# Optimization experiments

Hardware: AMD Instinct MI355X
Metric: run time of the kernel (lower is better)

## Reference

```python
import jax, jax.numpy as jnp
import numpy as np

D_MODEL = 1024
NUM_EXPERTS = 64
TOP_K = 2
TEMPERATURE = 1.0


def setup_inputs() -> dict:
    key = jax.random.key(0)
    k1, k2, k3, k4 = jax.random.split(key, 4)
    mh_output = jax.random.normal(k1, (8, 4096, D_MODEL), dtype=jnp.float32)
    noise = jax.random.normal(k2, (8, 4096, NUM_EXPERTS), dtype=jnp.float32)  # randn_like sample, externalized
    # nn.Linear weights: shape [out, in], init normal(0, 0.02); biases zero
    W_route = jax.random.normal(k3, (NUM_EXPERTS, D_MODEL), dtype=jnp.float32) * 0.02
    b_route = jnp.zeros((NUM_EXPERTS,), dtype=jnp.float32)
    W_noise = jax.random.normal(k4, (NUM_EXPERTS, D_MODEL), dtype=jnp.float32) * 0.02
    b_noise = jnp.zeros((NUM_EXPERTS,), dtype=jnp.float32)
    return {"mh_output": mh_output, "noise": noise, "W_route": W_route,
            "b_route": b_route, "W_noise": W_noise, "b_noise": b_noise}


def reference(mh_output, noise, W_route, b_route, W_noise, b_noise):
    # logits = topkroute_linear(mh_output); noise_logits = noise_linear(mh_output)
    logits = jnp.einsum('bsd,ed->bse', mh_output, W_route) + b_route
    noise_logits = jnp.einsum('bsd,ed->bse', mh_output, W_noise) + b_noise
    # noisy logits = logits + temperature * randn * softplus(noise_logits)
    noisy = logits + TEMPERATURE * noise * jax.nn.softplus(noise_logits)
    # top-k, scatter into -inf, softmax  ==  softmax over top-k values scattered into zeros
    top_vals, indices = jax.lax.top_k(noisy, TOP_K)          # [b, s, k]
    probs_k = jax.nn.softmax(top_vals, axis=-1)              # softmax(-inf elsewhere) -> 0 elsewhere
    one_hot = jax.nn.one_hot(indices, NUM_EXPERTS, dtype=noisy.dtype)  # [b, s, k, E]
    router_output = jnp.sum(one_hot * probs_k[..., None], axis=-2)     # [b, s, E]
    return router_output, indices
```

## Files before the change

### kernel.cpp

```cpp
#include <hip/hip_runtime.h>
#include <hip/hip_bf16.h>
#include <math.h>


#define T_TOKENS 32768
#define D_MODEL  1024
#define NE       64
#define NCOL     128
#define M_TILE   32
#define KSTAGE   64
#define NSTAGE   16
#define CS_LD    68
#define OUT_IDX_BASE ((size_t)T_TOKENS * NE)
#define W_ELEMS  (NCOL * D_MODEL)

typedef short  bf16x8  __attribute__((ext_vector_type(8)));
typedef float  floatx4 __attribute__((ext_vector_type(4)));

__device__ __forceinline__ float softplus_f(float x) {
    return fmaxf(x, 0.f) + log1pf(expf(-fabsf(x)));
}

__device__ __forceinline__ void cvt8(const float4 a, const float4 b,
                                     int4* hi, int4* lo) {
    float v[8] = {a.x, a.y, a.z, a.w, b.x, b.y, b.z, b.w};
    int hw[4], lw[4];
    #pragma unroll
    for (int p = 0; p < 4; ++p) {
        float2 f2 = make_float2(v[2 * p], v[2 * p + 1]);
        __hip_bfloat162 h2 = __float22bfloat162_rn(f2);
        int u; __builtin_memcpy(&u, &h2, 4);
        float h0 = __uint_as_float(((unsigned)u) << 16);
        float h1 = __uint_as_float(((unsigned)u) & 0xFFFF0000u);
        float2 l2 = make_float2(v[2 * p] - h0, v[2 * p + 1] - h1);
        __hip_bfloat162 L2 = __float22bfloat162_rn(l2);
        int ul; __builtin_memcpy(&ul, &L2, 4);
        hw[p] = u; lw[p] = ul;
    }
    *hi = make_int4(hw[0], hw[1], hw[2], hw[3]);
    *lo = make_int4(lw[0], lw[1], lw[2], lw[3]);
}

__global__ __launch_bounds__(256) void prepack_w(
    const float* __restrict__ Wr, const float* __restrict__ Wn,
    short* __restrict__ Bh, short* __restrict__ Bl)
{
    int g   = blockIdx.x * 256 + threadIdx.x;
    int n   = g & 15;
    int kg  = (g >> 4) & 127;
    int t2  = g >> 11;
    int col = t2 * 16 + n;
    const float* src = (col < NE ? Wr + (size_t)col * D_MODEL
                                 : Wn + (size_t)(col - NE) * D_MODEL) + kg * 8;
    float4 a = *(const float4*)src;
    float4 b = *(const float4*)(src + 4);
    int4 hi, lo;
    cvt8(a, b, &hi, &lo);
    *(int4*)(Bh + (size_t)g * 8) = hi;
    *(int4*)(Bl + (size_t)g * 8) = lo;
}

__global__ __launch_bounds__(256, 4) void router_mfma(
    const float* __restrict__ A,
    const float* __restrict__ noise,
    const float* __restrict__ br,
    const float* __restrict__ bn,
    const short* __restrict__ Bh,
    const short* __restrict__ Bl,
    float* __restrict__ out)
{
    __shared__ __align__(16) short Ah[2][M_TILE * KSTAGE];
    __shared__ __align__(16) short Al[2][M_TILE * KSTAGE];
    __shared__ float Cs[M_TILE * CS_LD];
    __shared__ float s_p1[M_TILE], s_p2[M_TILE];
    __shared__ int   s_e1[M_TILE], s_e2[M_TILE];

    const int tid  = threadIdx.x;
    const int lane = tid & 63;
    const int wid  = tid >> 6;
    const int n16  = lane & 15;
    const int quad = lane >> 4;
    const int m0   = blockIdx.x * M_TILE;

    const int r  = tid & 31;
    const int kh = tid >> 5;
    const float* pA = A + (size_t)(m0 + r) * D_MODEL + kh * 8;
    const int sBase = (kh * M_TILE + r) * 8;

    const int bBaseR = ((wid * 128 + quad) * 16 + n16) * 8;
    const int bBaseN = (((4 + wid) * 128 + quad) * 16 + n16) * 8;

    floatx4 acc[2][2];
    #pragma unroll
    for (int i = 0; i < 2; ++i) { acc[i][0] = (floatx4)0.f; acc[i][1] = (floatx4)0.f; }

    {
        float4 a0 = *(const float4*)pA;
        float4 a1 = *(const float4*)(pA + 4);
        int4 hi, lo;
        cvt8(a0, a1, &hi, &lo);
        *(int4*)&Ah[0][sBase] = hi;
        *(int4*)&Al[0][sBase] = lo;
    }
    float4 aP1a = *(const float4*)(pA + KSTAGE);
    float4 aP1b = *(const float4*)(pA + KSTAGE + 4);
    __syncthreads();

    for (int s = 0; s < NSTAGE; ++s) {
        const int cur = s & 1, nxt = cur ^ 1;

        float4 f0, f1;
        if (s + 2 < NSTAGE) {
            f0 = *(const float4*)(pA + (s + 2) * KSTAGE);
            f1 = *(const float4*)(pA + (s + 2) * KSTAGE + 4);
        }

        bf16x8 bh[2][2], bl[2][2];
        #pragma unroll
        for (int c = 0; c < 2; ++c) {
            const int o = (s * 2 + c) * 512;
            bh[c][0] = *(const bf16x8*)(Bh + bBaseR + o);
            bl[c][0] = *(const bf16x8*)(Bl + bBaseR + o);
            bh[c][1] = *(const bf16x8*)(Bh + bBaseN + o);
            bl[c][1] = *(const bf16x8*)(Bl + bBaseN + o);
        }

        bf16x8 afh[2][2], afl[2][2];
        #pragma unroll
        for (int c = 0; c < 2; ++c)
            #pragma unroll
            for (int mf = 0; mf < 2; ++mf) {
                int g = ((c * 4 + quad) * M_TILE + mf * 16 + n16) * 8;
                afh[c][mf] = *(const bf16x8*)&Ah[cur][g];
                afl[c][mf] = *(const bf16x8*)&Al[cur][g];
            }

        if (s + 1 < NSTAGE) {
            int4 hi, lo;
            cvt8(aP1a, aP1b, &hi, &lo);
            *(int4*)&Ah[nxt][sBase] = hi;
            *(int4*)&Al[nxt][sBase] = lo;
        }

        #pragma unroll
        for (int c = 0; c < 2; ++c)
            #pragma unroll
            for (int mf = 0; mf < 2; ++mf) {
                acc[mf][0] = __builtin_amdgcn_mfma_f32_16x16x32_bf16(afh[c][mf], bh[c][0], acc[mf][0], 0, 0, 0);
                acc[mf][0] = __builtin_amdgcn_mfma_f32_16x16x32_bf16(afh[c][mf], bl[c][0], acc[mf][0], 0, 0, 0);
                acc[mf][0] = __builtin_amdgcn_mfma_f32_16x16x32_bf16(afl[c][mf], bh[c][0], acc[mf][0], 0, 0, 0);
                acc[mf][1] = __builtin_amdgcn_mfma_f32_16x16x32_bf16(afh[c][mf], bh[c][1], acc[mf][1], 0, 0, 0);
                acc[mf][1] = __builtin_amdgcn_mfma_f32_16x16x32_bf16(afh[c][mf], bl[c][1], acc[mf][1], 0, 0, 0);
                acc[mf][1] = __builtin_amdgcn_mfma_f32_16x16x32_bf16(afl[c][mf], bh[c][1], acc[mf][1], 0, 0, 0);
            }

        __syncthreads();

        aP1a = f0; aP1b = f1;
    }

    {
        int e = wid * 16 + n16;
        float brv = br[e], bnv = bn[e];
        #pragma unroll
        for (int mf = 0; mf < 2; ++mf)
            #pragma unroll
            for (int rr = 0; rr < 4; ++rr) {
                int t = mf * 16 + quad * 4 + rr;
                float nz    = noise[(size_t)(m0 + t) * NE + e];
                float route = acc[mf][0][rr] + brv;
                float nl    = acc[mf][1][rr] + bnv;
                Cs[t * CS_LD + e] = fmaf(nz, softplus_f(nl), route);
            }
    }
    __syncthreads();

    if (tid < M_TILE) {
        const int t = tid;
        float v1 = -INFINITY, v2 = -INFINITY;
        int e1 = 0, e2 = 0;
        #pragma unroll
        for (int e4 = 0; e4 < 16; ++e4) {
            float4 q = *(const float4*)&Cs[t * CS_LD + e4 * 4];
            float qa[4] = {q.x, q.y, q.z, q.w};
            #pragma unroll
            for (int c = 0; c < 4; ++c) {
                float v = qa[c];
                int e = e4 * 4 + c;
                if (v > v1) { v2 = v1; e2 = e1; v1 = v; e1 = e; }
                else if (v > v2) { v2 = v; e2 = e; }
            }
        }
        float ex = expf(v2 - v1);
        float denom = 1.f + ex;
        s_p1[t] = 1.f / denom;
        s_p2[t] = ex / denom;
        s_e1[t] = e1;
        s_e2[t] = e2;
        float2 iv = make_float2((float)e1, (float)e2);
        *(float2*)(out + OUT_IDX_BASE + (size_t)(m0 + t) * 2) = iv;
    }
    __syncthreads();

    #pragma unroll
    for (int i = 0; i < 2; ++i) {
        int gi = i * 256 + tid;
        int t  = gi >> 4;
        int e0 = (gi & 15) * 4;
        float p1 = s_p1[t], p2 = s_p2[t];
        int   e1 = s_e1[t], e2 = s_e2[t];
        float4 v;
        v.x = (e0 + 0 == e1) ? p1 : ((e0 + 0 == e2) ? p2 : 0.f);
        v.y = (e0 + 1 == e1) ? p1 : ((e0 + 1 == e2) ? p2 : 0.f);
        v.z = (e0 + 2 == e1) ? p1 : ((e0 + 2 == e2) ? p2 : 0.f);
        v.w = (e0 + 3 == e1) ? p1 : ((e0 + 3 == e2) ? p2 : 0.f);
        *(float4*)(out + (size_t)(m0 + t) * NE + e0) = v;
    }
}

extern "C" void kernel_launch(void* const* d_in, const int* in_sizes, int n_in,
                              void* d_out, int out_size, void* d_ws, size_t ws_size,
                              hipStream_t stream) {
    const float* A     = (const float*)d_in[0];
    const float* noise = (const float*)d_in[1];
    const float* Wr    = (const float*)d_in[2];
    const float* br    = (const float*)d_in[3];
    const float* Wn    = (const float*)d_in[4];
    const float* bn    = (const float*)d_in[5];
    float* out = (float*)d_out;

    short* Bh = (short*)d_ws;
    short* Bl = Bh + W_ELEMS;

    prepack_w<<<dim3(W_ELEMS / 8 / 256), dim3(256), 0, stream>>>(Wr, Wn, Bh, Bl);
    router_mfma<<<dim3(T_TOKENS / M_TILE), dim3(256), 0, stream>>>(A, noise, br, bn, Bh, Bl, out);
}
```

Before: 231.7 us.

## Load A fragments directly into registers, dropping LDS staging and barriers

The main loop no longer stages activation tiles in shared memory. Each wave loads its own A fragments from global memory straight into the MFMA register layout, splits them into bf16 hi/lo in registers, and prefetches two chunks ahead. This removes the shared-memory writes and reads and the per-stage __syncthreads. In exchange, every one of the 4 waves now loads and converts the same A rows, so global/L2 traffic for A and the conversion ALU work both rise fourfold, and each thread's 32-byte loads are strided across rows, which is less coalesced.

```diff
diff --git a/kernel.cpp b/kernel.cpp
--- a/kernel.cpp
+++ b/kernel.cpp
@@ -8,8 +8,7 @@
 #define NE       64
 #define NCOL     128
 #define M_TILE   32
-#define KSTAGE   64
-#define NSTAGE   16
+#define NCHUNK   32
 #define CS_LD    68
 #define OUT_IDX_BASE ((size_t)T_TOKENS * NE)
 #define W_ELEMS  (NCOL * D_MODEL)
@@ -39,6 +38,14 @@
     }
     *hi = make_int4(hw[0], hw[1], hw[2], hw[3]);
     *lo = make_int4(lw[0], lw[1], lw[2], lw[3]);
+}
+
+__device__ __forceinline__ void cvt8r(const float4 a, const float4 b,
+                                      bf16x8* hi, bf16x8* lo) {
+    int4 h, l;
+    cvt8(a, b, &h, &l);
+    __builtin_memcpy(hi, &h, 16);
+    __builtin_memcpy(lo, &l, 16);
 }
 
 __global__ __launch_bounds__(256) void prepack_w(
@@ -69,8 +76,6 @@
     const short* __restrict__ Bl,
     float* __restrict__ out)
 {
-    __shared__ __align__(16) short Ah[2][M_TILE * KSTAGE];
-    __shared__ __align__(16) short Al[2][M_TILE * KSTAGE];
     __shared__ float Cs[M_TILE * CS_LD];
     __shared__ float s_p1[M_TILE], s_p2[M_TILE];
     __shared__ int   s_e1[M_TILE], s_e2[M_TILE];
@@ -82,81 +87,63 @@
     const int quad = lane >> 4;
     const int m0   = blockIdx.x * M_TILE;
 
-    const int r  = tid & 31;
-    const int kh = tid >> 5;
-    const float* pA = A + (size_t)(m0 + r) * D_MODEL + kh * 8;
-    const int sBase = (kh * M_TILE + r) * 8;
-
-    const int bBaseR = ((wid * 128 + quad) * 16 + n16) * 8;
-    const int bBaseN = (((4 + wid) * 128 + quad) * 16 + n16) * 8;
+    const float* pA0 = A + (size_t)(m0 + n16) * D_MODEL + quad * 8;
+    const float* pA1 = pA0 + (size_t)16 * D_MODEL;
+
+    const short* pBhR = Bh + ((size_t)(wid * 128 + quad) * 16 + n16) * 8;
+    const short* pBlR = Bl + ((size_t)(wid * 128 + quad) * 16 + n16) * 8;
+    const short* pBhN = Bh + ((size_t)((4 + wid) * 128 + quad) * 16 + n16) * 8;
+    const short* pBlN = Bl + ((size_t)((4 + wid) * 128 + quad) * 16 + n16) * 8;
 
     floatx4 acc[2][2];
     #pragma unroll
     for (int i = 0; i < 2; ++i) { acc[i][0] = (floatx4)0.f; acc[i][1] = (floatx4)0.f; }
 
-    {
-        float4 a0 = *(const float4*)pA;
-        float4 a1 = *(const float4*)(pA + 4);
-        int4 hi, lo;
-        cvt8(a0, a1, &hi, &lo);
-        *(int4*)&Ah[0][sBase] = hi;
-        *(int4*)&Al[0][sBase] = lo;
-    }
-    float4 aP1a = *(const float4*)(pA + KSTAGE);
-    float4 aP1b = *(const float4*)(pA + KSTAGE + 4);
-    __syncthreads();
-
-    for (int s = 0; s < NSTAGE; ++s) {
-        const int cur = s & 1, nxt = cur ^ 1;
-
-        float4 f0, f1;
-        if (s + 2 < NSTAGE) {
-            f0 = *(const float4*)(pA + (s + 2) * KSTAGE);
-            f1 = *(const float4*)(pA + (s + 2) * KSTAGE + 4);
+    float4 c0a = *(const float4*)(pA0);
+    float4 c0b = *(const float4*)(pA0 + 4);
+    float4 c1a = *(const float4*)(pA1);
+    float4 c1b = *(const float4*)(pA1 + 4);
+    float4 n0a = *(const float4*)(pA0 + 32);
+    float4 n0b = *(const float4*)(pA0 + 36);
+    float4 n1a = *(const float4*)(pA1 + 32);
+    float4 n1b = *(const float4*)(pA1 + 36);
+
+    for (int kc = 0; kc < NCHUNK; ++kc) {
+        float4 t0a, t0b, t1a, t1b;
+        if (kc + 2 < NCHUNK) {
+            const float* q0 = pA0 + (kc + 2) * 32;
+            const float* q1 = pA1 + (kc + 2) * 32;
+            t0a = *(const float4*)(q0);
+            t0b = *(const float4*)(q0 + 4);
+            t1a = *(const float4*)(q1);
+            t1b = *(const float4*)(q1 + 4);
         }
 
-        bf16x8 bh[2][2], bl[2][2];
-        #pragma unroll
-        for (int c = 0; c < 2; ++c) {
-            const int o = (s * 2 + c) * 512;
-            bh[c][0] = *(const bf16x8*)(Bh + bBaseR + o);
-            bl[c][0] = *(const bf16x8*)(Bl + bBaseR + o);
-            bh[c][1] = *(const bf16x8*)(Bh + bBaseN + o);
-            bl[c][1] = *(const bf16x8*)(Bl + bBaseN + o);
-        }
-
-        bf16x8 afh[2][2], afl[2][2];
-        #pragma unroll
-        for (int c = 0; c < 2; ++c)
-            #pragma unroll
-            for (int mf = 0; mf < 2; ++mf) {
-                int g = ((c * 4 + quad) * M_TILE + mf * 16 + n16) * 8;
-                afh[c][mf] = *(const bf16x8*)&Ah[cur][g];
-                afl[c][mf] = *(const bf16x8*)&Al[cur][g];
-            }
-
-        if (s + 1 < NSTAGE) {
-            int4 hi, lo;
-            cvt8(aP1a, aP1b, &hi, &lo);
-            *(int4*)&Ah[nxt][sBase] = hi;
-            *(int4*)&Al[nxt][sBase] = lo;
-        }
-
-        #pragma unroll
-        for (int c = 0; c < 2; ++c)
-            #pragma unroll
-            for (int mf = 0; mf < 2; ++mf) {
-                acc[mf][0] = __builtin_amdgcn_mfma_f32_16x16x32_bf16(afh[c][mf], bh[c][0], acc[mf][0], 0, 0, 0);
-                acc[mf][0] = __builtin_amdgcn_mfma_f32_16x16x32_bf16(afh[c][mf], bl[c][0], acc[mf][0], 0, 0, 0);
-                acc[mf][0] = __builtin_amdgcn_mfma_f32_16x16x32_bf16(afl[c][mf], bh[c][0], acc[mf][0], 0, 0, 0);
-                acc[mf][1] = __builtin_amdgcn_mfma_f32_16x16x32_bf16(afh[c][mf], bh[c][1], acc[mf][1], 0, 0, 0);
-                acc[mf][1] = __builtin_amdgcn_mfma_f32_16x16x32_bf16(afh[c][mf], bl[c][1], acc[mf][1], 0, 0, 0);
-                acc[mf][1] = __builtin_amdgcn_mfma_f32_16x16x32_bf16(afl[c][mf], bh[c][1], acc[mf][1], 0, 0, 0);
-            }
-
-        __syncthreads();
-
-        aP1a = f0; aP1b = f1;
+        const int o = kc * 512;
+        bf16x8 bhR = *(const bf16x8*)(pBhR + o);
+        bf16x8 blR = *(const bf16x8*)(pBlR + o);
+        bf16x8 bhN = *(const bf16x8*)(pBhN + o);
+        bf16x8 blN = *(const bf16x8*)(pBlN + o);
+
+        bf16x8 ah0, al0, ah1, al1;
+        cvt8r(c0a, c0b, &ah0, &al0);
+        cvt8r(c1a, c1b, &ah1, &al1);
+
+        acc[0][0] = __builtin_amdgcn_mfma_f32_16x16x32_bf16(ah0, bhR, acc[0][0], 0, 0, 0);
+        acc[0][0] = __builtin_amdgcn_mfma_f32_16x16x32_bf16(ah0, blR, acc[0][0], 0, 0, 0);
+        acc[0][0] = __builtin_amdgcn_mfma_f32_16x16x32_bf16(al0, bhR, acc[0][0], 0, 0, 0);
+        acc[0][1] = __builtin_amdgcn_mfma_f32_16x16x32_bf16(ah0, bhN, acc[0][1], 0, 0, 0);
+        acc[0][1] = __builtin_amdgcn_mfma_f32_16x16x32_bf16(ah0, blN, acc[0][1], 0, 0, 0);
+        acc[0][1] = __builtin_amdgcn_mfma_f32_16x16x32_bf16(al0, bhN, acc[0][1], 0, 0, 0);
+        acc[1][0] = __builtin_amdgcn_mfma_f32_16x16x32_bf16(ah1, bhR, acc[1][0], 0, 0, 0);
+        acc[1][0] = __builtin_amdgcn_mfma_f32_16x16x32_bf16(ah1, blR, acc[1][0], 0, 0, 0);
+        acc[1][0] = __builtin_amdgcn_mfma_f32_16x16x32_bf16(al1, bhR, acc[1][0], 0, 0, 0);
+        acc[1][1] = __builtin_amdgcn_mfma_f32_16x16x32_bf16(ah1, bhN, acc[1][1], 0, 0, 0);
+        acc[1][1] = __builtin_amdgcn_mfma_f32_16x16x32_bf16(ah1, blN, acc[1][1], 0, 0, 0);
+        acc[1][1] = __builtin_amdgcn_mfma_f32_16x16x32_bf16(al1, bhN, acc[1][1], 0, 0, 0);
+
+        c0a = n0a; c0b = n0b; c1a = n1a; c1b = n1b;
+        n0a = t0a; n0b = t0b; n1a = t1a; n1b = t1b;
     }
 
     {
```

Result: slower. 261.3 us (+12.8%).

## Double token tile to 64, prefetch B fragments and noise, spread top-k across waves

Applied to the files above, without the earlier changes.

Raises the per-block token tile from 32 to 64, so each B-fragment load from global memory feeds four M-fragments instead of two, halving the weight traffic per token. B fragments for the next stage are loaded into registers one iteration ahead, and the noise values are loaded early (at stage NSTAGE-3) so their latency hides behind the MFMA loop. The top-k pass now uses 16 lanes in each of the four waves instead of the first 32 threads. The cost is more registers and LDS per block, with launch bounds lowered from 4 to 2 blocks per SM, so occupancy drops.

```diff
diff --git a/kernel.cpp b/kernel.cpp
--- a/kernel.cpp
+++ b/kernel.cpp
@@ -7,7 +7,7 @@
 #define D_MODEL  1024
 #define NE       64
 #define NCOL     128
-#define M_TILE   32
+#define M_TILE   64
 #define KSTAGE   64
 #define NSTAGE   16
 #define CS_LD    68
@@ -60,7 +60,7 @@
     *(int4*)(Bl + (size_t)g * 8) = lo;
 }
 
-__global__ __launch_bounds__(256, 4) void router_mfma(
+__global__ __launch_bounds__(256, 2) void router_mfma(
     const float* __restrict__ A,
     const float* __restrict__ noise,
     const float* __restrict__ br,
@@ -82,101 +82,139 @@
     const int quad = lane >> 4;
     const int m0   = blockIdx.x * M_TILE;
 
-    const int r  = tid & 31;
-    const int kh = tid >> 5;
-    const float* pA = A + (size_t)(m0 + r) * D_MODEL + kh * 8;
-    const int sBase = (kh * M_TILE + r) * 8;
-
-    const int bBaseR = ((wid * 128 + quad) * 16 + n16) * 8;
-    const int bBaseN = (((4 + wid) * 128 + quad) * 16 + n16) * 8;
-
-    floatx4 acc[2][2];
+    const int r  = tid & 63;
+    const int g  = tid >> 6;
+    const float* pA = A + (size_t)(m0 + r) * D_MODEL + g * 8;
+    const int sBase = (g * M_TILE + r) * 8;
+
+    const short* pBhR = Bh + ((size_t)(wid * 128 + quad) * 16 + n16) * 8;
+    const short* pBlR = Bl + ((size_t)(wid * 128 + quad) * 16 + n16) * 8;
+    const short* pBhN = Bh + ((size_t)((4 + wid) * 128 + quad) * 16 + n16) * 8;
+    const short* pBlN = Bl + ((size_t)((4 + wid) * 128 + quad) * 16 + n16) * 8;
+
+    floatx4 acc[4][2];
     #pragma unroll
-    for (int i = 0; i < 2; ++i) { acc[i][0] = (floatx4)0.f; acc[i][1] = (floatx4)0.f; }
+    for (int i = 0; i < 4; ++i) { acc[i][0] = (floatx4)0.f; acc[i][1] = (floatx4)0.f; }
 
     {
-        float4 a0 = *(const float4*)pA;
+        float4 a0 = *(const float4*)(pA);
         float4 a1 = *(const float4*)(pA + 4);
+        float4 a2 = *(const float4*)(pA + 32);
+        float4 a3 = *(const float4*)(pA + 36);
         int4 hi, lo;
         cvt8(a0, a1, &hi, &lo);
         *(int4*)&Ah[0][sBase] = hi;
         *(int4*)&Al[0][sBase] = lo;
-    }
-    float4 aP1a = *(const float4*)(pA + KSTAGE);
-    float4 aP1b = *(const float4*)(pA + KSTAGE + 4);
+        cvt8(a2, a3, &hi, &lo);
+        *(int4*)&Ah[0][sBase + 2048] = hi;
+        *(int4*)&Al[0][sBase + 2048] = lo;
+    }
+    float4 nx0a = *(const float4*)(pA + KSTAGE);
+    float4 nx0b = *(const float4*)(pA + KSTAGE + 4);
+    float4 nx1a = *(const float4*)(pA + KSTAGE + 32);
+    float4 nx1b = *(const float4*)(pA + KSTAGE + 36);
+    bf16x8 c0hR = *(const bf16x8*)(pBhR);
+    bf16x8 c0lR = *(const bf16x8*)(pBlR);
+    bf16x8 c0hN = *(const bf16x8*)(pBhN);
+    bf16x8 c0lN = *(const bf16x8*)(pBlN);
     __syncthreads();
 
+    float nz[4][4];
+
+    #pragma unroll 2
     for (int s = 0; s < NSTAGE; ++s) {
         const int cur = s & 1, nxt = cur ^ 1;
 
-        float4 f0, f1;
+        float4 f0a, f0b, f1a, f1b;
         if (s + 2 < NSTAGE) {
-            f0 = *(const float4*)(pA + (s + 2) * KSTAGE);
-            f1 = *(const float4*)(pA + (s + 2) * KSTAGE + 4);
-        }
-
-        bf16x8 bh[2][2], bl[2][2];
-        #pragma unroll
-        for (int c = 0; c < 2; ++c) {
-            const int o = (s * 2 + c) * 512;
-            bh[c][0] = *(const bf16x8*)(Bh + bBaseR + o);
-            bl[c][0] = *(const bf16x8*)(Bl + bBaseR + o);
-            bh[c][1] = *(const bf16x8*)(Bh + bBaseN + o);
-            bl[c][1] = *(const bf16x8*)(Bl + bBaseN + o);
-        }
-
-        bf16x8 afh[2][2], afl[2][2];
-        #pragma unroll
-        for (int c = 0; c < 2; ++c)
+            const float* q = pA + (s + 2) * KSTAGE;
+            f0a = *(const float4*)(q);
+            f0b = *(const float4*)(q + 4);
+            f1a = *(const float4*)(q + 32);
+            f1b = *(const float4*)(q + 36);
+        }
+
+        const int ob1 = (s * 2 + 1) * 512;
+        bf16x8 c1hR = *(const bf16x8*)(pBhR + ob1);
+        bf16x8 c1lR = *(const bf16x8*)(pBlR + ob1);
+        bf16x8 c1hN = *(const bf16x8*)(pBhN + ob1);
+        bf16x8 c1lN = *(const bf16x8*)(pBlN + ob1);
+        bf16x8 n0hR, n0lR, n0hN, n0lN;
+        if (s + 1 < NSTAGE) {
+            const int ob0 = (s + 1) * 2 * 512;
+            n0hR = *(const bf16x8*)(pBhR + ob0);
+            n0lR = *(const bf16x8*)(pBlR + ob0);
+            n0hN = *(const bf16x8*)(pBhN + ob0);
+            n0lN = *(const bf16x8*)(pBlN + ob0);
+        }
+
+        if (s == NSTAGE - 3) {
+            const int e = wid * 16 + n16;
             #pragma unroll
-            for (int mf = 0; mf < 2; ++mf) {
-                int g = ((c * 4 + quad) * M_TILE + mf * 16 + n16) * 8;
-                afh[c][mf] = *(const bf16x8*)&Ah[cur][g];
-                afl[c][mf] = *(const bf16x8*)&Al[cur][g];
-            }
+            for (int mf = 0; mf < 4; ++mf)
+                #pragma unroll
+                for (int rr = 0; rr < 4; ++rr)
+                    nz[mf][rr] = noise[(size_t)(m0 + mf * 16 + quad * 4 + rr) * NE + e];
+        }
+
+        #pragma unroll
+        for (int mf = 0; mf < 4; ++mf) {
+            const int gi = (quad * M_TILE + mf * 16 + n16) * 8;
+            bf16x8 afh = *(const bf16x8*)&Ah[cur][gi];
+            bf16x8 afl = *(const bf16x8*)&Al[cur][gi];
+            acc[mf][0] = __builtin_amdgcn_mfma_f32_16x16x32_bf16(afh, c0hR, acc[mf][0], 0, 0, 0);
+            acc[mf][0] = __builtin_amdgcn_mfma_f32_16x16x32_bf16(afh, c0lR, acc[mf][0], 0, 0, 0);
+            acc[mf][0] = __builtin_amdgcn_mfma_f32_16x16x32_bf16(afl, c0hR, acc[mf][0], 0, 0, 0);
+            acc[mf][1] = __builtin_amdgcn_mfma_f32_16x16x32_bf16(afh, c0hN, acc[mf][1], 0, 0, 0);
+            acc[mf][1] = __builtin_amdgcn_mfma_f32_16x16x32_bf16(afh, c0lN, acc[mf][1], 0, 0, 0);
+            acc[mf][1] = __builtin_amdgcn_mfma_f32_16x16x32_bf16(afl, c0hN, acc[mf][1], 0, 0, 0);
+        }
+        #pragma unroll
+        for (int mf = 0; mf < 4; ++mf) {
+            const int gi = ((4 + quad) * M_TILE + mf * 16 + n16) * 8;
+            bf16x8 afh = *(const bf16x8*)&Ah[cur][gi];
+            bf16x8 afl = *(const bf16x8*)&Al[cur][gi];
+            acc[mf][0] = __builtin_amdgcn_mfma_f32_16x16x32_bf16(afh, c1hR, acc[mf][0], 0, 0, 0);
+            acc[mf][0] = __builtin_amdgcn_mfma_f32_16x16x32_bf16(afh, c1lR, acc[mf][0], 0, 0, 0);
+            acc[mf][0] = __builtin_amdgcn_mfma_f32_16x16x32_bf16(afl, c1hR, acc[mf][0], 0, 0, 0);
+            acc[mf][1] = __builtin_amdgcn_mfma_f32_16x16x32_bf16(afh, c1hN, acc[mf][1], 0, 0, 0);
+            acc[mf][1] = __builtin_amdgcn_mfma_f32_16x16x32_bf16(afh, c1lN, acc[mf][1], 0, 0, 0);
+            acc[mf][1] = __builtin_amdgcn_mfma_f32_16x16x32_bf16(afl, c1hN, acc[mf][1], 0, 0, 0);
+        }
 
         if (s + 1 < NSTAGE) {
             int4 hi, lo;
-            cvt8(aP1a, aP1b, &hi, &lo);
+            cvt8(nx0a, nx0b, &hi, &lo);
             *(int4*)&Ah[nxt][sBase] = hi;
             *(int4*)&Al[nxt][sBase] = lo;
-        }
-
-        #pragma unroll
-        for (int c = 0; c < 2; ++c)
-            #pragma unroll
-            for (int mf = 0; mf < 2; ++mf) {
-                acc[mf][0] = __builtin_amdgcn_mfma_f32_16x16x32_bf16(afh[c][mf], bh[c][0], acc[mf][0], 0, 0, 0);
-                acc[mf][0] = __builtin_amdgcn_mfma_f32_16x16x32_bf16(afh[c][mf], bl[c][0], acc[mf][0], 0, 0, 0);
-                acc[mf][0] = __builtin_amdgcn_mfma_f32_16x16x32_bf16(afl[c][mf], bh[c][0], acc[mf][0], 0, 0, 0);
-                acc[mf][1] = __builtin_amdgcn_mfma_f32_16x16x32_bf16(afh[c][mf], bh[c][1], acc[mf][1], 0, 0, 0);
-                acc[mf][1] = __builtin_amdgcn_mfma_f32_16x16x32_bf16(afh[c][mf], bl[c][1], acc[mf][1], 0, 0, 0);
-                acc[mf][1] = __builtin_amdgcn_mfma_f32_16x16x32_bf16(afl[c][mf], bh[c][1], acc[mf][1], 0, 0, 0);
-            }
+            cvt8(nx1a, nx1b, &hi, &lo);
+            *(int4*)&Ah[nxt][sBase + 2048] = hi;
+            *(int4*)&Al[nxt][sBase + 2048] = lo;
+        }
 
         __syncthreads();
 
-        aP1a = f0; aP1b = f1;
+        nx0a = f0a; nx0b = f0b; nx1a = f1a; nx1b = f1b;
+        c0hR = n0hR; c0lR = n0lR; c0hN = n0hN; c0lN = n0lN;
     }
 
     {
-        int e = wid * 16 + n16;
+        const int e = wid * 16 + n16;
         float brv = br[e], bnv = bn[e];
         #pragma unroll
-        for (int mf = 0; mf < 2; ++mf)
+        for (int mf = 0; mf < 4; ++mf)
             #pragma unroll
             for (int rr = 0; rr < 4; ++rr) {
                 int t = mf * 16 + quad * 4 + rr;
-                float nz    = noise[(size_t)(m0 + t) * NE + e];
                 float route = acc[mf][0][rr] + brv;
                 float nl    = acc[mf][1][rr] + bnv;
-                Cs[t * CS_LD + e] = fmaf(nz, softplus_f(nl), route);
+                Cs[t * CS_LD + e] = fmaf(nz[mf][rr], softplus_f(nl), route);
             }
     }
     __syncthreads();
 
-    if (tid < M_TILE) {
-        const int t = tid;
+    if (lane < 16) {
+        const int t = wid * 16 + lane;
         float v1 = -INFINITY, v2 = -INFINITY;
         int e1 = 0, e2 = 0;
         #pragma unroll
@@ -203,7 +241,7 @@
     __syncthreads();
 
     #pragma unroll
-    for (int i = 0; i < 2; ++i) {
+    for (int i = 0; i < 4; ++i) {
         int gi = i * 256 + tid;
         int t  = gi >> 4;
         int e0 = (gi & 15) * 4;
```

Result: no change. 230.1 us (-0.7%).
